# Optimization experiments

Hardware: AMD Instinct MI355X
Metric: run time of the kernel (lower is better)

The kernel has to match this reference:

```python
import jax, jax.numpy as jnp
import numpy as np

B, L, DH = 8, 4096, 1024
T, DG, P = 1024, 768, 256
EPS = 1e-8


def setup_inputs() -> dict:
    key = jax.random.key(0)
    k1, k2, k3, k4 = jax.random.split(key, 4)
    H = jax.random.normal(k1, (B, L, DH), dtype=jnp.float32)
    G = jax.random.normal(k2, (B, T, DG), dtype=jnp.float32)
    # nn.Linear(d, P, bias=False) weights: shape [P, d], uniform(-1/sqrt(d), 1/sqrt(d))
    Wq = jax.random.uniform(k3, (P, DG), jnp.float32, -1.0, 1.0) / jnp.sqrt(jnp.float32(DG))
    Wk = jax.random.uniform(k4, (P, DH), jnp.float32, -1.0, 1.0) / jnp.sqrt(jnp.float32(DH))
    return {"H": H, "G": G, "Wq": Wq, "Wk": Wk}


def reference(H, G, Wq, Wk):
    # Chunked online-softmax streaming is mathematically equivalent to one
    # full stable softmax cross-attention pass; values are the raw H.
    scale = jnp.float32(P) ** -0.5
    Q = jnp.einsum("btd,pd->btp", G, Wq)          # [B,T,P]
    K = jnp.einsum("bld,pd->blp", H, Wk)          # [B,L,P]
    logits = jnp.einsum("btp,blp->btl", Q, K).astype(jnp.float32) * scale
    m = jnp.max(logits, axis=-1, keepdims=True)
    p = jnp.exp(logits - m)                        # [B,T,L]
    s = jnp.sum(p, axis=-1, keepdims=True)         # [B,T,1]
    z = jnp.einsum("btl,bld->btd", p, H.astype(jnp.float32))
    Z = (z / (s + EPS)).astype(H.dtype)            # [B,T,DH]
    return Z
```

## Files before the change

### kernel.cpp

```cpp
#include <hip/hip_runtime.h>
#include <hip/hip_bf16.h>
#include <stdint.h>

#define Bn  8
#define Ln  4096
#define DHn 1024
#define Tn  1024
#define DGn 768
#define Pn  256

typedef float  f32x4  __attribute__((ext_vector_type(4)));
typedef __bf16 bf16x8 __attribute__((ext_vector_type(8)));

__device__ __forceinline__ void gload16(const void* g, void* l) {
  __builtin_amdgcn_global_load_lds(
      (const __attribute__((address_space(1))) void*)g,
      (__attribute__((address_space(3))) void*)l, 16, 0, 0);
}

__device__ __forceinline__ unsigned short f2bf(float x) {
  union { float f; uint32_t u; } v; v.f = x;
  uint32_t u = v.u;
  return (unsigned short)((u + 0x7FFFu + ((u >> 16) & 1u)) >> 16);
}

__device__ __forceinline__ float bf2f(unsigned short b) {
  union { uint32_t u; float f; } v; v.u = ((uint32_t)b) << 16;
  return v.f;
}

__global__ void cvt_kernel(const float4* __restrict__ in,
                           ushort4* __restrict__ out, int n4) {
  int i = blockIdx.x * 256 + threadIdx.x;
  if (i < n4) {
    float4 v = in[i];
    ushort4 o;
    o.x = f2bf(v.x); o.y = f2bf(v.y); o.z = f2bf(v.z); o.w = f2bf(v.w);
    out[i] = o;
  }
}

__global__ void prep_H(const float* __restrict__ Hg,
                       unsigned short* __restrict__ Hb,
                       unsigned short* __restrict__ HT) {
  __shared__ unsigned short tile[64 * 65];
  const int b  = blockIdx.z;
  const int l0 = blockIdx.x * 64;
  const int d0 = blockIdx.y * 64;
  const float4* src  = (const float4*)(Hg + (size_t)b * Ln * DHn);
  ushort4*      dstH = (ushort4*)(Hb + (size_t)b * Ln * DHn);
  for (int e = threadIdx.x; e < 1024; e += 256) {
    int l  = e >> 4;
    int d4 = e & 15;
    size_t idx4 = ((size_t)(l0 + l) * DHn + d0) / 4 + d4;
    float4 v = src[idx4];
    ushort4 o;
    o.x = f2bf(v.x); o.y = f2bf(v.y); o.z = f2bf(v.z); o.w = f2bf(v.w);
    dstH[idx4] = o;
    int d = d4 * 4;
    tile[(d + 0) * 65 + l] = o.x;
    tile[(d + 1) * 65 + l] = o.y;
    tile[(d + 2) * 65 + l] = o.z;
    tile[(d + 3) * 65 + l] = o.w;
  }
  __syncthreads();
  ushort4* dst = (ushort4*)(HT + (size_t)b * DHn * Ln);
  for (int e = threadIdx.x; e < 1024; e += 256) {
    int d  = e >> 4;
    int l4 = (e & 15) * 4;
    ushort4 o;
    o.x = tile[d * 65 + l4 + 0];
    o.y = tile[d * 65 + l4 + 1];
    o.z = tile[d * 65 + l4 + 2];
    o.w = tile[d * 65 + l4 + 3];
    dst[((size_t)(d0 + d) * Ln + l0) / 4 + (e & 15)] = o;
  }
}

template <int EPI>
__global__ __launch_bounds__(256) void gemm_bt(
    const unsigned short* __restrict__ A, const unsigned short* __restrict__ B,
    void* __restrict__ Cout, float* __restrict__ S,
    int kLen, int lda, int ldb, int ldc,
    long sA, long sB, long sC, int sS, float scale, int mTiles, int nTiles) {
  __shared__ unsigned short As[128 * 32];
  __shared__ unsigned short Bs[128 * 32];
  int x = blockIdx.x;
  const int b = x & (Bn - 1);
  int r = x >> 3;
  const int ni = r % nTiles; r /= nTiles;
  const int mi = r % mTiles;
  const int ks = r / mTiles;
  const unsigned short* Ab = A + (long)b * sA;
  const unsigned short* Bb = B + (long)b * sB;
  const int m0 = mi * 128;
  const int n0 = ni * 128;
  const int kBeg = ks * kLen;
  const int tid  = threadIdx.x;
  const int lane = tid & 63;
  const int wave = tid >> 6;
  const int wm = (wave >> 1) << 6;
  const int wn = (wave & 1) << 6;
  const int lrow = lane & 15;
  const int quad = lane >> 4;
  const int srow0 = lane >> 2;
  const int skcol = (lane & 3) << 3;

  f32x4 acc[4][4];
#pragma unroll
  for (int mt = 0; mt < 4; ++mt)
#pragma unroll
    for (int nt = 0; nt < 4; ++nt) acc[mt][nt] = f32x4{0.f, 0.f, 0.f, 0.f};

  for (int k0 = kBeg; k0 < kBeg + kLen; k0 += 32) {
    __syncthreads();
#pragma unroll
    for (int j = 0; j < 2; ++j) {
      int c = wave * 2 + j;
      int row = c * 16 + srow0;
      gload16(Ab + (size_t)(m0 + row) * lda + (k0 + skcol), &As[c * 512]);
      gload16(Bb + (size_t)(n0 + row) * ldb + (k0 + skcol), &Bs[c * 512]);
    }
    __syncthreads();
    bf16x8 af[4], bfr[4];
#pragma unroll
    for (int mt = 0; mt < 4; ++mt)
      af[mt] = *(const bf16x8*)&As[(wm + mt * 16 + lrow) * 32 + quad * 8];
#pragma unroll
    for (int nt = 0; nt < 4; ++nt)
      bfr[nt] = *(const bf16x8*)&Bs[(wn + nt * 16 + lrow) * 32 + quad * 8];
#pragma unroll
    for (int mt = 0; mt < 4; ++mt)
#pragma unroll
      for (int nt = 0; nt < 4; ++nt)
        acc[mt][nt] = __builtin_amdgcn_mfma_f32_16x16x32_bf16(
            af[mt], bfr[nt], acc[mt][nt], 0, 0, 0);
  }

  if (EPI == 0) {
    unsigned short* C = (unsigned short*)Cout + (long)b * sC;
#pragma unroll
    for (int mt = 0; mt < 4; ++mt)
#pragma unroll
      for (int r2 = 0; r2 < 4; ++r2) {
        int row = m0 + wm + mt * 16 + quad * 4 + r2;
        unsigned short* Cr = C + (size_t)row * ldc + n0 + wn + lrow;
#pragma unroll
        for (int nt = 0; nt < 4; ++nt) Cr[nt * 16] = f2bf(acc[mt][nt][r2]);
      }
  } else if (EPI == 1) {
    unsigned short* C = (unsigned short*)Cout + (long)b * sC;
    float* Sb = S + (long)b * sS;
#pragma unroll
    for (int mt = 0; mt < 4; ++mt)
#pragma unroll
      for (int r2 = 0; r2 < 4; ++r2) {
        int row = m0 + wm + mt * 16 + quad * 4 + r2;
        unsigned short* Cr = C + (size_t)row * ldc + n0 + wn + lrow;
        float psum = 0.f;
#pragma unroll
        for (int nt = 0; nt < 4; ++nt) {
          float e = __expf(acc[mt][nt][r2] * scale);
          unsigned short bv = f2bf(e);
          Cr[nt * 16] = bv;
          psum += bf2f(bv);
        }
        psum += __shfl_xor(psum, 1);
        psum += __shfl_xor(psum, 2);
        psum += __shfl_xor(psum, 4);
        psum += __shfl_xor(psum, 8);
        if (lrow == 0) atomicAdd(&Sb[row], psum);
      }
  } else {
    float* C = (float*)Cout + (long)b * sC;
    const float* Sb = S + (long)b * sS;
#pragma unroll
    for (int mt = 0; mt < 4; ++mt)
#pragma unroll
      for (int r2 = 0; r2 < 4; ++r2) {
        int row = m0 + wm + mt * 16 + quad * 4 + r2;
        float inv = 1.f / (Sb[row] + 1e-8f);
        float* Cr = C + (size_t)row * ldc + n0 + wn + lrow;
#pragma unroll
        for (int nt = 0; nt < 4; ++nt) {
          if (EPI == 2) Cr[nt * 16] = acc[mt][nt][r2] * inv;
          else          atomicAdd(&Cr[nt * 16], acc[mt][nt][r2] * inv);
        }
      }
  }
}

extern "C" void kernel_launch(void* const* d_in, const int* in_sizes, int n_in,
                              void* d_out, int out_size, void* d_ws, size_t ws_size,
                              hipStream_t stream) {
  const float* H  = (const float*)d_in[0];
  const float* G  = (const float*)d_in[1];
  const float* Wq = (const float*)d_in[2];
  const float* Wk = (const float*)d_in[3];
  float* out = (float*)d_out;

  char* ws = (char*)d_ws;
  size_t off = 0;
  auto alloc = [&](size_t bytes) {
    void* p = ws + off;
    off = (off + bytes + 255) & ~(size_t)255;
    return p;
  };
  unsigned short* Hb  = (unsigned short*)alloc((size_t)Bn * Ln * DHn * 2);
  unsigned short* HbT = (unsigned short*)alloc((size_t)Bn * DHn * Ln * 2);
  unsigned short* Gb  = (unsigned short*)alloc((size_t)Bn * Tn * DGn * 2);
  unsigned short* Wqb = (unsigned short*)alloc((size_t)Pn * DGn * 2);
  unsigned short* Wkb = (unsigned short*)alloc((size_t)Pn * DHn * 2);
  unsigned short* Kb  = (unsigned short*)alloc((size_t)Bn * Ln * Pn * 2);
  unsigned short* Qb  = (unsigned short*)alloc((size_t)Bn * Tn * Pn * 2);
  float* Sv           = (float*)alloc((size_t)Bn * Tn * 4);
  unsigned short* Pm = Hb;

  {
    int n4 = Bn * Tn * DGn / 4;
    cvt_kernel<<<(n4 + 255) / 256, 256, 0, stream>>>((const float4*)G, (ushort4*)Gb, n4);
  }
  {
    int n4 = Pn * DGn / 4;
    cvt_kernel<<<(n4 + 255) / 256, 256, 0, stream>>>((const float4*)Wq, (ushort4*)Wqb, n4);
  }
  {
    int n4 = Pn * DHn / 4;
    cvt_kernel<<<(n4 + 255) / 256, 256, 0, stream>>>((const float4*)Wk, (ushort4*)Wkb, n4);
  }
  prep_H<<<dim3(Ln / 64, DHn / 64, Bn), 256, 0, stream>>>(H, Hb, HbT);
  hipMemsetAsync(Sv, 0, (size_t)Bn * Tn * 4, stream);
  hipMemsetAsync(out, 0, (size_t)Bn * Tn * DHn * 4, stream);

  gemm_bt<0><<<Bn * 32 * 2, 256, 0, stream>>>(
      Hb, Wkb, Kb, nullptr, DHn, DHn, DHn, Pn,
      (long)Ln * DHn, 0L, (long)Ln * Pn, 0, 1.f, 32, 2);
  gemm_bt<0><<<Bn * 8 * 2, 256, 0, stream>>>(
      Gb, Wqb, Qb, nullptr, DGn, DGn, DGn, Pn,
      (long)Tn * DGn, 0L, (long)Tn * Pn, 0, 1.f, 8, 2);
  gemm_bt<1><<<Bn * 8 * 32, 256, 0, stream>>>(
      Qb, Kb, Pm, Sv, Pn, Pn, Pn, Ln,
      (long)Tn * Pn, (long)Ln * Pn, (long)Tn * Ln, Tn, 0.0625f, 8, 32);
  gemm_bt<3><<<Bn * 8 * 8 * 2, 256, 0, stream>>>(
      Pm, HbT, out, Sv, Ln / 2, Ln, Ln, DHn,
      (long)Tn * Ln, (long)DHn * Ln, (long)Tn * DHn, Tn, 1.f, 8, 8);
}
```

Baseline: 507.5 us.

## Swizzle GEMM LDS tiles and replace split-K atomics with partial buffers

XOR-swizzles the 16-byte chunk position within each LDS row, applied both to the global-to-LDS loads and to the MFMA fragment reads, to cut bank conflicts. The split-K P·H GEMM now writes each K-half's raw fp32 result to its own buffer: the output, or a scratch region reusing the dead G/K/Q workspace. The float atomicAdds and the output memset are dropped. A new elementwise kernel sums the two partials and applies the 1/(S+eps) normalization, at the cost of an extra launch and a full read/write pass over the output.

After: 474.6 us. 1.07x faster.

```diff
diff --git a/kernel.cpp b/kernel.cpp
--- a/kernel.cpp
+++ b/kernel.cpp
@@ -80,7 +80,7 @@
 template <int EPI>
 __global__ __launch_bounds__(256) void gemm_bt(
     const unsigned short* __restrict__ A, const unsigned short* __restrict__ B,
-    void* __restrict__ Cout, float* __restrict__ S,
+    void* __restrict__ Cout, void* __restrict__ CoutB, float* __restrict__ S,
     int kLen, int lda, int ldb, int ldc,
     long sA, long sB, long sC, int sS, float scale, int mTiles, int nTiles) {
   __shared__ unsigned short As[128 * 32];
@@ -104,7 +104,8 @@
   const int lrow = lane & 15;
   const int quad = lane >> 4;
   const int srow0 = lane >> 2;
-  const int skcol = (lane & 3) << 3;
+  const int skcol = (((lane & 3) ^ ((srow0 >> 1) & 3)) << 3);
+  const int fslot = (quad ^ ((lrow >> 1) & 3)) << 3;
 
   f32x4 acc[4][4];
 #pragma unroll
@@ -125,10 +126,10 @@
     bf16x8 af[4], bfr[4];
 #pragma unroll
     for (int mt = 0; mt < 4; ++mt)
-      af[mt] = *(const bf16x8*)&As[(wm + mt * 16 + lrow) * 32 + quad * 8];
+      af[mt] = *(const bf16x8*)&As[(wm + mt * 16 + lrow) * 32 + fslot];
 #pragma unroll
     for (int nt = 0; nt < 4; ++nt)
-      bfr[nt] = *(const bf16x8*)&Bs[(wn + nt * 16 + lrow) * 32 + quad * 8];
+      bfr[nt] = *(const bf16x8*)&Bs[(wn + nt * 16 + lrow) * 32 + fslot];
 #pragma unroll
     for (int mt = 0; mt < 4; ++mt)
 #pragma unroll
@@ -171,7 +172,7 @@
         psum += __shfl_xor(psum, 8);
         if (lrow == 0) atomicAdd(&Sb[row], psum);
       }
-  } else {
+  } else if (EPI == 2) {
     float* C = (float*)Cout + (long)b * sC;
     const float* Sb = S + (long)b * sS;
 #pragma unroll
@@ -182,11 +183,37 @@
         float inv = 1.f / (Sb[row] + 1e-8f);
         float* Cr = C + (size_t)row * ldc + n0 + wn + lrow;
 #pragma unroll
-        for (int nt = 0; nt < 4; ++nt) {
-          if (EPI == 2) Cr[nt * 16] = acc[mt][nt][r2] * inv;
-          else          atomicAdd(&Cr[nt * 16], acc[mt][nt][r2] * inv);
-        }
-      }
+        for (int nt = 0; nt < 4; ++nt) Cr[nt * 16] = acc[mt][nt][r2] * inv;
+      }
+  } else {
+    float* C = (float*)(ks == 0 ? Cout : CoutB) + (long)b * sC;
+#pragma unroll
+    for (int mt = 0; mt < 4; ++mt)
+#pragma unroll
+      for (int r2 = 0; r2 < 4; ++r2) {
+        int row = m0 + wm + mt * 16 + quad * 4 + r2;
+        float* Cr = C + (size_t)row * ldc + n0 + wn + lrow;
+#pragma unroll
+        for (int nt = 0; nt < 4; ++nt) Cr[nt * 16] = acc[mt][nt][r2];
+      }
+  }
+}
+
+__global__ void reduce_norm(float4* __restrict__ out,
+                            const float4* __restrict__ p1,
+                            const float* __restrict__ S, int n4) {
+  int i = blockIdx.x * 256 + threadIdx.x;
+  if (i < n4) {
+    int row = i >> 8;
+    float inv = 1.f / (S[row] + 1e-8f);
+    float4 a = out[i];
+    float4 c = p1[i];
+    float4 o;
+    o.x = (a.x + c.x) * inv;
+    o.y = (a.y + c.y) * inv;
+    o.z = (a.z + c.z) * inv;
+    o.w = (a.w + c.w) * inv;
+    out[i] = o;
   }
 }
 
@@ -215,6 +242,7 @@
   unsigned short* Qb  = (unsigned short*)alloc((size_t)Bn * Tn * Pn * 2);
   float* Sv           = (float*)alloc((size_t)Bn * Tn * 4);
   unsigned short* Pm = Hb;
+  float* Part1 = (float*)Gb;
 
   {
     int n4 = Bn * Tn * DGn / 4;
@@ -230,18 +258,22 @@
   }
   prep_H<<<dim3(Ln / 64, DHn / 64, Bn), 256, 0, stream>>>(H, Hb, HbT);
   hipMemsetAsync(Sv, 0, (size_t)Bn * Tn * 4, stream);
-  hipMemsetAsync(out, 0, (size_t)Bn * Tn * DHn * 4, stream);
 
   gemm_bt<0><<<Bn * 32 * 2, 256, 0, stream>>>(
-      Hb, Wkb, Kb, nullptr, DHn, DHn, DHn, Pn,
+      Hb, Wkb, Kb, nullptr, nullptr, DHn, DHn, DHn, Pn,
       (long)Ln * DHn, 0L, (long)Ln * Pn, 0, 1.f, 32, 2);
   gemm_bt<0><<<Bn * 8 * 2, 256, 0, stream>>>(
-      Gb, Wqb, Qb, nullptr, DGn, DGn, DGn, Pn,
+      Gb, Wqb, Qb, nullptr, nullptr, DGn, DGn, DGn, Pn,
       (long)Tn * DGn, 0L, (long)Tn * Pn, 0, 1.f, 8, 2);
   gemm_bt<1><<<Bn * 8 * 32, 256, 0, stream>>>(
-      Qb, Kb, Pm, Sv, Pn, Pn, Pn, Ln,
+      Qb, Kb, Pm, nullptr, Sv, Pn, Pn, Pn, Ln,
       (long)Tn * Pn, (long)Ln * Pn, (long)Tn * Ln, Tn, 0.0625f, 8, 32);
   gemm_bt<3><<<Bn * 8 * 8 * 2, 256, 0, stream>>>(
-      Pm, HbT, out, Sv, Ln / 2, Ln, Ln, DHn,
-      (long)Tn * Ln, (long)DHn * Ln, (long)Tn * DHn, Tn, 1.f, 8, 8);
-}
+      Pm, HbT, out, Part1, nullptr, Ln / 2, Ln, Ln, DHn,
+      (long)Tn * Ln, (long)DHn * Ln, (long)Tn * DHn, 0, 1.f, 8, 8);
+  {
+    int n4 = Bn * Tn * DHn / 4;
+    reduce_norm<<<(n4 + 255) / 256, 256, 0, stream>>>(
+        (float4*)out, (const float4*)Part1, Sv, n4);
+  }
+}
```
